# Kernel optimization log

Hardware: AMD Instinct MI355X
Metric: run time of the kernel (lower is better)

Reference implementation:

```python
import jax, jax.numpy as jnp
import numpy as np

NUM_HEADS = 16
ROPE_BASE = 10000.0
LN_EPS = 1e-5


def _rope_tables(seq_len, head_dim, dtype):
    # half-dim angle table: (seq_len, head_dim//2)
    inv_freq = 1.0 / (ROPE_BASE ** (jnp.arange(0, head_dim, 2, dtype=jnp.float32) / head_dim))
    angles = jnp.arange(seq_len, dtype=jnp.float32)[:, None] * inv_freq[None, :]
    return jnp.cos(angles).astype(dtype), jnp.sin(angles).astype(dtype)


def _apply_rope(x, cos, sin):
    # x: (B, H, S, D_h); rotate interleaved (even, odd) dim pairs
    xe = x[..., 0::2]
    xo = x[..., 1::2]
    c = cos[None, None, :, :]
    s = sin[None, None, :, :]
    re = xe * c - xo * s
    ro = xe * s + xo * c
    return jnp.stack([re, ro], axis=-1).reshape(x.shape)


def _layernorm(x, g, b):
    mu = jnp.mean(x, axis=-1, keepdims=True)
    var = jnp.var(x, axis=-1, keepdims=True)
    return (x - mu) * jax.lax.rsqrt(var + LN_EPS) * g + b


def setup_inputs() -> dict:
    key = jax.random.key(0)
    ks = jax.random.split(key, 8)
    B, S, D, F = 2, 2048, 1024, 4096
    sd = lambda fan_in: 1.0 / np.sqrt(fan_in)
    return {
        "x": jax.random.normal(ks[0], (B, S, D), jnp.float32),
        "in_proj_w": jax.random.normal(ks[1], (3 * D, D), jnp.float32) * sd(D),
        "in_proj_b": jnp.zeros((3 * D,), jnp.float32),
        "out_w": jax.random.normal(ks[2], (D, D), jnp.float32) * sd(D),
        "out_b": jnp.zeros((D,), jnp.float32),
        "w1": jax.random.normal(ks[3], (F, D), jnp.float32) * sd(D),
        "b1": jnp.zeros((F,), jnp.float32),
        "w2": jax.random.normal(ks[4], (D, F), jnp.float32) * sd(F),
        "b2": jnp.zeros((D,), jnp.float32),
        "ln1_g": jnp.ones((D,), jnp.float32),
        "ln1_b": jnp.zeros((D,), jnp.float32),
        "ln2_g": jnp.ones((D,), jnp.float32),
        "ln2_b": jnp.zeros((D,), jnp.float32),
    }


def reference(x, in_proj_w, in_proj_b, out_w, out_b, w1, b1, w2, b2,
              ln1_g, ln1_b, ln2_g, ln2_b):
    B, S, D = x.shape
    H = NUM_HEADS
    Dh = D // H
    scale = Dh ** -0.5

    # fused QKV projection
    qkv = x @ in_proj_w.T + in_proj_b  # (B, S, 3D)
    q, k, v = jnp.split(qkv, 3, axis=-1)
    q = q.reshape(B, S, H, Dh).transpose(0, 2, 1, 3)
    k = k.reshape(B, S, H, Dh).transpose(0, 2, 1, 3)
    v = v.reshape(B, S, H, Dh).transpose(0, 2, 1, 3)

    cos, sin = _rope_tables(S, Dh, x.dtype)
    q = _apply_rope(q, cos, sin)
    k = _apply_rope(k, cos, sin)

    # SDPA (no mask, no dropout)
    scores = jnp.einsum('bhqd,bhkd->bhqk', q, k) * scale
    probs = jax.nn.softmax(scores, axis=-1)
    attn = jnp.einsum('bhqk,bhkd->bhqd', probs, v)
    attn = attn.transpose(0, 2, 1, 3).reshape(B, S, D)
    attn_out = attn @ out_w.T + out_b

    # post-norm encoder layer: residual + LN, FFN, residual + LN
    h = _layernorm(x + attn_out, ln1_g, ln1_b)
    ff = jax.nn.relu(h @ w1.T + b1) @ w2.T + b2
    return _layernorm(h + ff, ln2_g, ln2_b)
```

## Files before the change

kernel.cpp:

```cpp
#include <hip/hip_runtime.h>
#include <math.h>

typedef unsigned short u16;
typedef unsigned int u32;
typedef __attribute__((ext_vector_type(8))) __bf16 bf16x8;
typedef __attribute__((ext_vector_type(4))) float f32x4;

#define AS1 __attribute__((address_space(1)))
#define AS3 __attribute__((address_space(3)))

#define B_ 2
#define S_ 2048
#define D_ 1024
#define H_ 16
#define DH_ 64
#define F_ 4096
#define M_ 4096

__device__ __forceinline__ u16 f2b(float f) {
  u32 u = __builtin_bit_cast(u32, f);
  u += 0x7fffu + ((u >> 16) & 1u);
  return (u16)(u >> 16);
}

__device__ __forceinline__ u32 pack2(float a, float b) {
  u16 lo = __builtin_bit_cast(u16, (__bf16)a);
  u16 hi = __builtin_bit_cast(u16, (__bf16)b);
  return (u32)lo | ((u32)hi << 16);
}

__global__ __launch_bounds__(256) void cvt_kernel(const float* __restrict__ in,
                                                  u16* __restrict__ out, int n4) {
  int i = blockIdx.x * 256 + threadIdx.x;
  if (i < n4) {
    float4 v = ((const float4*)in)[i];
    ushort4 o;
    o.x = f2b(v.x); o.y = f2b(v.y); o.z = f2b(v.z); o.w = f2b(v.w);
    ((ushort4*)out)[i] = o;
  }
}

__global__ __launch_bounds__(256) void tables_kernel(float* __restrict__ cosT,
                                                     float* __restrict__ sinT) {
  int idx = blockIdx.x * 256 + threadIdx.x;
  int s = idx >> 5, i = idx & 31;
  float inv = powf(10000.0f, -(float)i / 32.0f);
  float ang = (float)s * inv;
  cosT[idx] = cosf(ang);
  sinT[idx] = sinf(ang);
}

template <bool BIAS, bool RELU, bool SPLIT, typename OutT>
__global__ __launch_bounds__(256) void gemm_bt(const u16* __restrict__ A,
                                               const u16* __restrict__ Bm,
                                               const float* __restrict__ bias,
                                               OutT* __restrict__ C, int M, int N, int K,
                                               int kChunk) {
  __shared__ u16 sA[128 * 32];
  __shared__ u16 sB[128 * 32];
  const int t = threadIdx.x;
  const int w = t >> 6, lane = t & 63;
  const int fr = lane & 15, fg = lane >> 4;
  const int row0 = blockIdx.y * 128, col0 = blockIdx.x * 128;
  const int wr = (w >> 1) * 64, wc = (w & 1) * 64;

  f32x4 acc[4][4] = {};

  const int rA = t >> 2;
  const int jj = ((t & 3) ^ ((t >> 3) & 3)) << 4;
  const int rdswz = ((fg ^ ((fr >> 1) & 3)) << 4);
  const char* aRead = (const char*)sA + (wr + fr) * 64 + rdswz;
  const char* bRead = (const char*)sB + (wc + fr) * 64 + rdswz;

  const int kb = blockIdx.z * kChunk;
  for (int k0 = kb; k0 < kb + kChunk; k0 += 32) {
#pragma unroll
    for (int i = 0; i < 2; ++i) {
      const char* srcA = (const char*)(A + (size_t)(row0 + i * 64 + rA) * K + k0) + jj;
      const char* srcB = (const char*)(Bm + (size_t)(col0 + i * 64 + rA) * K + k0) + jj;
      char* dA = (char*)sA + i * 4096 + w * 1024;
      char* dB = (char*)sB + i * 4096 + w * 1024;
      __builtin_amdgcn_global_load_lds((const AS1 u32*)srcA, (AS3 u32*)dA, 16, 0, 0);
      __builtin_amdgcn_global_load_lds((const AS1 u32*)srcB, (AS3 u32*)dB, 16, 0, 0);
    }
    __syncthreads();

    bf16x8 af[4], bfr[4];
#pragma unroll
    for (int m = 0; m < 4; ++m) af[m] = *(const bf16x8*)(aRead + m * 1024);
#pragma unroll
    for (int n = 0; n < 4; ++n) bfr[n] = *(const bf16x8*)(bRead + n * 1024);
#pragma unroll
    for (int m = 0; m < 4; ++m)
#pragma unroll
      for (int n = 0; n < 4; ++n)
        acc[m][n] = __builtin_amdgcn_mfma_f32_16x16x32_bf16(af[m], bfr[n], acc[m][n], 0, 0, 0);
    __syncthreads();
  }

  OutT* Cp = C;
  if constexpr (SPLIT) Cp = C + (size_t)blockIdx.z * M * N;
#pragma unroll
  for (int m = 0; m < 4; ++m) {
    const int rowb = row0 + wr + m * 16 + fg * 4;
#pragma unroll
    for (int n = 0; n < 4; ++n) {
      const int col = col0 + wc + n * 16 + fr;
      float bv = BIAS ? bias[col] : 0.0f;
      f32x4 c = acc[m][n];
#pragma unroll
      for (int r = 0; r < 4; ++r) {
        float v = c[r] + bv;
        if (RELU) v = fmaxf(v, 0.0f);
        if constexpr (sizeof(OutT) == 2)
          ((u16*)Cp)[(size_t)(rowb + r) * N + col] = f2b(v);
        else
          ((float*)Cp)[(size_t)(rowb + r) * N + col] = v;
      }
    }
  }
}

__global__ __launch_bounds__(256) void rope_kernel(const u16* __restrict__ qkv,
                                                   const float* __restrict__ cosT,
                                                   const float* __restrict__ sinT,
                                                   u16* __restrict__ qr, u16* __restrict__ kr,
                                                   u16* __restrict__ vt) {
  const int bh = blockIdx.x;
  const int b = bh >> 4, h = bh & 15;
  const int s0 = blockIdx.y * 64;
  const int t = threadIdx.x;

#pragma unroll
  for (int part = 0; part < 2; ++part) {
    const u16* src = qkv + (size_t)(b * S_ + s0) * (3 * D_) + part * D_ + h * DH_;
    u16* dst = (part ? kr : qr) + ((size_t)bh * S_ + s0) * DH_;
    const float psc = part ? 1.0f : 0.125f * 1.44269504088896340736f;
    for (int it = 0; it < 8; ++it) {
      int item = it * 256 + t;
      int sl = item >> 5, i = item & 31;
      u32 v = *(const u32*)(src + (size_t)sl * (3 * D_) + 2 * i);
      float xe = __builtin_bit_cast(float, v << 16);
      float xo = __builtin_bit_cast(float, v & 0xffff0000u);
      int s = s0 + sl;
      float c = cosT[s * 32 + i], sn = sinT[s * 32 + i];
      float re = (xe * c - xo * sn) * psc;
      float ro = (xe * sn + xo * c) * psc;
      *(u32*)(dst + (size_t)sl * DH_ + 2 * i) = pack2(re, ro);
    }
  }

  __shared__ u16 tile[64][65];
  const u16* vsrc = qkv + (size_t)(b * S_ + s0) * (3 * D_) + 2 * D_ + h * DH_;
  for (int it = 0; it < 16; ++it) {
    int sl = it * 4 + (t >> 6), dh = t & 63;
    tile[sl][dh] = vsrc[(size_t)sl * (3 * D_) + dh];
  }
  __syncthreads();
  u16* vdst = vt + (size_t)bh * DH_ * S_ + s0;
  for (int it = 0; it < 16; ++it) {
    int dh = it * 4 + (t >> 6), sl = t & 63;
    vdst[(size_t)dh * S_ + sl] = tile[sl][dh];
  }
}

__global__ __launch_bounds__(256) void attn_kernel(const u16* __restrict__ qr,
                                                   const u16* __restrict__ kr,
                                                   const u16* __restrict__ vt,
                                                   u16* __restrict__ attn) {
  __shared__ u16 sK[2][64 * 64];
  __shared__ u16 sV[2][64 * 64];
  __shared__ u16 plds[4][1024];
  const int bh = blockIdx.x;
  const int b = bh >> 4, h = bh & 15;
  const int q0 = blockIdx.y * 64;
  const int t = threadIdx.x, w = t >> 6, lane = t & 63;
  const int fr = lane & 15, fg = lane >> 4;

  const int qrow = q0 + w * 16 + fr;
  const u16* qbase = qr + ((size_t)bh * S_ + qrow) * DH_;
  bf16x8 qf0 = *(const bf16x8*)(qbase + fg * 8);
  bf16x8 qf1 = *(const bf16x8*)(qbase + 32 + fg * 8);

  const char* kByte = (const char*)(kr + (size_t)bh * S_ * DH_);
  const char* vByte = (const char*)(vt + (size_t)bh * DH_ * S_);
  char* pbase = (char*)&plds[w][0];
  const int ci0 = w * 64 + lane;

  f32x4 oacc[4] = {};
  float psum_acc = 0.0f;
  const float M0 = 12.0f;

  auto stage = [&](int bufb, int kt) {
#pragma unroll
    for (int i = 0; i < 2; ++i) {
      int ci = i * 256 + ci0;
      int r = ci >> 3, j = ci & 7;
      int jj = j ^ (r & 7);
      const char* srcK = kByte + (size_t)(kt + r) * 128 + (jj << 4);
      const char* srcV = vByte + (size_t)r * (S_ * 2) + (size_t)kt * 2 + (jj << 4);
      char* dK = (char*)&sK[bufb][0] + i * 4096 + w * 1024;
      char* dV = (char*)&sV[bufb][0] + i * 4096 + w * 1024;
      __builtin_amdgcn_global_load_lds((const AS1 u32*)srcK, (AS3 u32*)dK, 16, 0, 0);
      __builtin_amdgcn_global_load_lds((const AS1 u32*)srcV, (AS3 u32*)dV, 16, 0, 0);
    }
  };

  stage(0, 0);
  __syncthreads();

  int buf = 0;
  for (int kt = 0; kt < S_; kt += 64) {
    if (kt + 64 < S_) stage(buf ^ 1, kt + 64);

    const char* kB = (const char*)&sK[buf][0];
    const char* vB = (const char*)&sV[buf][0];

    f32x4 st[4];
    __builtin_amdgcn_s_setprio(1);
#pragma unroll
    for (int ks = 0; ks < 4; ++ks) {
      const char* rowp = kB + (ks * 16 + fr) * 128;
      bf16x8 kf0 = *(const bf16x8*)(rowp + ((fg ^ (fr & 7)) << 4));
      bf16x8 kf1 = *(const bf16x8*)(rowp + (((fg + 4) ^ (fr & 7)) << 4));
      f32x4 z = {};
      z = __builtin_amdgcn_mfma_f32_16x16x32_bf16(kf0, qf0, z, 0, 0, 0);
      st[ks] = __builtin_amdgcn_mfma_f32_16x16x32_bf16(kf1, qf1, z, 0, 0, 0);
    }
    __builtin_amdgcn_s_setprio(0);

#pragma unroll
    for (int ks = 0; ks < 4; ++ks) {
      float p0 = __builtin_amdgcn_exp2f(st[ks][0] - M0);
      float p1 = __builtin_amdgcn_exp2f(st[ks][1] - M0);
      float p2 = __builtin_amdgcn_exp2f(st[ks][2] - M0);
      float p3 = __builtin_amdgcn_exp2f(st[ks][3] - M0);
      psum_acc += (p0 + p1) + (p2 + p3);
      int wb = fr * 128 + (((ks * 32) | (fg * 8)) ^ ((fr & 7) << 4));
      *(uint2*)(pbase + wb) = make_uint2(pack2(p0, p1), pack2(p2, p3));
    }

    asm volatile("s_waitcnt lgkmcnt(0)" ::: "memory");
    __builtin_amdgcn_sched_barrier(0);

    __builtin_amdgcn_s_setprio(1);
#pragma unroll
    for (int ksub = 0; ksub < 2; ++ksub) {
      int rb = fr * 128 + (((ksub * 64) | (fg * 16)) ^ ((fr & 7) << 4));
      bf16x8 pf = *(const bf16x8*)(pbase + rb);
#pragma unroll
      for (int d = 0; d < 4; ++d) {
        const char* vp = vB + (d * 16 + fr) * 128 + ((((ksub * 4) | fg) ^ (fr & 7)) << 4);
        bf16x8 vf = *(const bf16x8*)vp;
        oacc[d] = __builtin_amdgcn_mfma_f32_16x16x32_bf16(vf, pf, oacc[d], 0, 0, 0);
      }
    }
    __builtin_amdgcn_s_setprio(0);
    __syncthreads();
    buf ^= 1;
  }

  psum_acc += __shfl_xor(psum_acc, 16);
  psum_acc += __shfl_xor(psum_acc, 32);
  const float inv_l = 1.0f / psum_acc;
  u16* obase = attn + (size_t)(b * S_ + q0 + w * 16 + fr) * D_ + h * DH_;
#pragma unroll
  for (int d = 0; d < 4; ++d) {
    ushort4 o4;
    o4.x = f2b(oacc[d][0] * inv_l);
    o4.y = f2b(oacc[d][1] * inv_l);
    o4.z = f2b(oacc[d][2] * inv_l);
    o4.w = f2b(oacc[d][3] * inv_l);
    *(ushort4*)(obase + d * 16 + fg * 4) = o4;
  }
}

template <int NS, bool WRITE_BF16>
__global__ __launch_bounds__(256) void reduce_ln_kernel(const float* __restrict__ parts,
                                                        const float* __restrict__ bias,
                                                        const float* __restrict__ resid,
                                                        const float* __restrict__ gamma,
                                                        const float* __restrict__ beta,
                                                        float* __restrict__ outf,
                                                        u16* __restrict__ outb) {
  const int row = blockIdx.x;
  const int t = threadIdx.x;
  const size_t base = (size_t)row * D_;
  float4 v = ((const float4*)bias)[t];
  {
    const float4 r4 = ((const float4*)(resid + base))[t];
    v.x += r4.x; v.y += r4.y; v.z += r4.z; v.w += r4.w;
  }
#pragma unroll
  for (int s = 0; s < NS; ++s) {
    const float4 p4 = ((const float4*)(parts + (size_t)s * M_ * D_ + base))[t];
    v.x += p4.x; v.y += p4.y; v.z += p4.z; v.w += p4.w;
  }
  float s = v.x + v.y + v.z + v.w;
  float ss = v.x * v.x + v.y * v.y + v.z * v.z + v.w * v.w;
#pragma unroll
  for (int off = 1; off < 64; off <<= 1) {
    s += __shfl_xor(s, off);
    ss += __shfl_xor(ss, off);
  }
  __shared__ float red[8];
  const int w = t >> 6, lane = t & 63;
  if (lane == 0) { red[w] = s; red[4 + w] = ss; }
  __syncthreads();
  s = red[0] + red[1] + red[2] + red[3];
  ss = red[4] + red[5] + red[6] + red[7];
  const float mu = s * (1.0f / D_);
  const float var = ss * (1.0f / D_) - mu * mu;
  const float rstd = rsqrtf(var + 1e-5f);
  const float4 g4 = ((const float4*)gamma)[t];
  const float4 b4 = ((const float4*)beta)[t];
  float4 o;
  o.x = (v.x - mu) * rstd * g4.x + b4.x;
  o.y = (v.y - mu) * rstd * g4.y + b4.y;
  o.z = (v.z - mu) * rstd * g4.z + b4.z;
  o.w = (v.w - mu) * rstd * g4.w + b4.w;
  ((float4*)(outf + base))[t] = o;
  if constexpr (WRITE_BF16) {
    ushort4 ob;
    ob.x = f2b(o.x); ob.y = f2b(o.y); ob.z = f2b(o.z); ob.w = f2b(o.w);
    ((ushort4*)(outb + base))[t] = ob;
  }
}

extern "C" void kernel_launch(void* const* d_in, const int* in_sizes, int n_in,
                              void* d_out, int out_size, void* d_ws, size_t ws_size,
                              hipStream_t stream) {
  const float* x = (const float*)d_in[0];
  const float* in_proj_w = (const float*)d_in[1];
  const float* in_proj_b = (const float*)d_in[2];
  const float* out_w = (const float*)d_in[3];
  const float* out_b = (const float*)d_in[4];
  const float* w1 = (const float*)d_in[5];
  const float* b1 = (const float*)d_in[6];
  const float* w2 = (const float*)d_in[7];
  const float* b2 = (const float*)d_in[8];
  const float* ln1_g = (const float*)d_in[9];
  const float* ln1_b = (const float*)d_in[10];
  const float* ln2_g = (const float*)d_in[11];
  const float* ln2_b = (const float*)d_in[12];

  char* ws = (char*)d_ws;
  u16* wib = (u16*)(ws + 0);
  u16* wob = (u16*)(ws + 6291456);
  u16* w1b = (u16*)(ws + 8388608);
  u16* w2b = (u16*)(ws + 16777216);
  float* cosT = (float*)(ws + 25165824);
  float* sinT = (float*)(ws + 25427968);
  u16* qkvb = (u16*)(ws + 25690112);
  float* part = (float*)(ws + 25690112);
  u16* qrb = (u16*)(ws + 59244544);
  u16* krb = (u16*)(ws + 67633152);
  u16* vtb = (u16*)(ws + 76021760);
  u16* attnb = (u16*)(ws + 84410368);
  u16* ff = (u16*)(ws + 59244544);
  u16* xb = (u16*)(ws + 92798976);
  float* hf = (float*)(ws + 92798976);
  u16* hb = (u16*)(ws + 109576192);
  (void)ws_size; (void)in_sizes; (void)n_in; (void)out_size;

  cvt_kernel<<<4096, 256, 0, stream>>>(x, xb, 1048576);
  cvt_kernel<<<3072, 256, 0, stream>>>(in_proj_w, wib, 786432);
  cvt_kernel<<<1024, 256, 0, stream>>>(out_w, wob, 262144);
  cvt_kernel<<<4096, 256, 0, stream>>>(w1, w1b, 1048576);
  cvt_kernel<<<4096, 256, 0, stream>>>(w2, w2b, 1048576);
  tables_kernel<<<256, 256, 0, stream>>>(cosT, sinT);

  gemm_bt<true, false, false, u16><<<dim3(24, 32), 256, 0, stream>>>(
      xb, wib, in_proj_b, qkvb, M_, 3 * D_, D_, D_);

  rope_kernel<<<dim3(32, 32), 256, 0, stream>>>(qkvb, cosT, sinT, qrb, krb, vtb);

  attn_kernel<<<dim3(32, 32), 256, 0, stream>>>(qrb, krb, vtb, attnb);

  gemm_bt<false, false, true, float><<<dim3(8, 32, 2), 256, 0, stream>>>(
      attnb, wob, nullptr, part, M_, D_, D_, 512);
  reduce_ln_kernel<2, true><<<4096, 256, 0, stream>>>(part, out_b, x, ln1_g, ln1_b, hf, hb);

  gemm_bt<true, true, false, u16><<<dim3(32, 32), 256, 0, stream>>>(
      hb, w1b, b1, ff, M_, F_, D_, D_);

  gemm_bt<false, false, true, float><<<dim3(8, 32, 2), 256, 0, stream>>>(
      ff, w2b, nullptr, part, M_, D_, F_, 2048);
  reduce_ln_kernel<2, false><<<4096, 256, 0, stream>>>(part, b2, hf, ln2_g, ln2_b,
                                                       (float*)d_out, nullptr);
}
```

Baseline: 394.7 us.

## Add 256x256 double-buffered direct-to-LDS GEMM for QKV and FFN1 projections

```diff
diff --git a/kernel.cpp b/kernel.cpp
--- a/kernel.cpp
+++ b/kernel.cpp
@@ -48,6 +48,116 @@
   float ang = (float)s * inv;
   cosT[idx] = cosf(ang);
   sinT[idx] = sinf(ang);
+}
+
+template <bool RELU>
+__global__ __launch_bounds__(512, 2) void gemm256(const u16* __restrict__ A,
+                                                  const u16* __restrict__ Bm,
+                                                  const float* __restrict__ bias,
+                                                  u16* __restrict__ C, int M, int N, int K) {
+  __shared__ u16 sA[2][256 * 64];
+  __shared__ u16 sB[2][256 * 64];
+  const int t = threadIdx.x;
+  const int w = t >> 6, lane = t & 63;
+  const int fr = lane & 15, fg = lane >> 4;
+  const int wm = w >> 2, wn = w & 3;
+
+  const int nwg = gridDim.x * gridDim.y;
+  const int bid = blockIdx.y * gridDim.x + blockIdx.x;
+  const int swz = (bid & 7) * (nwg >> 3) + (bid >> 3);
+  const int bx = swz % gridDim.x, by = swz / gridDim.x;
+  const int row0 = by * 256, col0 = bx * 256;
+
+  f32x4 acc[8][4] = {};
+
+  auto stage_part = [&](int bf, int kt, int p) {
+    const u16* gsrc = (p & 2) ? Bm : A;
+    const int blk0 = (p & 2) ? col0 : row0;
+    u16(*dstT)[256 * 64] = (p & 2) ? sB : sA;
+#pragma unroll
+    for (int l = 0; l < 2; ++l) {
+      int idx = (w * 2 + l) * 64 + lane;
+      int r = ((p & 1) << 7) + (idx >> 3);
+      int j = idx & 7;
+      const char* src = (const char*)(gsrc + (size_t)(blk0 + r) * K + kt * 64) +
+                        (((j ^ (r & 7)) << 4));
+      char* dst = (char*)&dstT[bf][0] + ((p & 1) << 14) + (w * 2 + l) * 1024;
+      __builtin_amdgcn_global_load_lds((const AS1 u32*)src, (AS3 u32*)dst, 16, 0, 0);
+    }
+  };
+
+  const int NT = K >> 6;
+#pragma unroll
+  for (int p = 0; p < 4; ++p) stage_part(0, 0, p);
+
+  int bufc = 0;
+  for (int kt = 0; kt < NT; ++kt) {
+    const int nx = bufc ^ 1;
+    bf16x8 bfr[4][2];
+#pragma unroll
+    for (int ph = 0; ph < 4; ++ph) {
+      if (ph == 0) {
+        if (kt + 1 < NT) {
+          stage_part(nx, kt + 1, 0);
+          asm volatile("s_waitcnt vmcnt(2)" ::: "memory");
+        } else {
+          asm volatile("s_waitcnt vmcnt(0)" ::: "memory");
+        }
+        __builtin_amdgcn_s_barrier();
+        __builtin_amdgcn_sched_barrier(0);
+#pragma unroll
+        for (int n = 0; n < 4; ++n)
+#pragma unroll
+          for (int kh = 0; kh < 2; ++kh) {
+            int br = wn * 64 + n * 16 + fr;
+            bfr[n][kh] = *(const bf16x8*)((const char*)&sB[bufc][0] + br * 128 +
+                                          (((kh * 4 + fg) ^ (br & 7)) << 4));
+          }
+      } else {
+        if (kt + 1 < NT) stage_part(nx, kt + 1, ph);
+      }
+      bf16x8 af[2][2];
+#pragma unroll
+      for (int mm = 0; mm < 2; ++mm)
+#pragma unroll
+        for (int kh = 0; kh < 2; ++kh) {
+          int ar = wm * 128 + (ph * 2 + mm) * 16 + fr;
+          af[mm][kh] = *(const bf16x8*)((const char*)&sA[bufc][0] + ar * 128 +
+                                        (((kh * 4 + fg) ^ (ar & 7)) << 4));
+        }
+      if (ph != 0) __builtin_amdgcn_s_barrier();
+      __builtin_amdgcn_s_setprio(1);
+#pragma unroll
+      for (int mm = 0; mm < 2; ++mm)
+#pragma unroll
+        for (int n = 0; n < 4; ++n)
+#pragma unroll
+          for (int kh = 0; kh < 2; ++kh)
+            acc[ph * 2 + mm][n] = __builtin_amdgcn_mfma_f32_16x16x32_bf16(
+                af[mm][kh], bfr[n][kh], acc[ph * 2 + mm][n], 0, 0, 0);
+      __builtin_amdgcn_s_setprio(0);
+      __builtin_amdgcn_s_barrier();
+    }
+    bufc = nx;
+  }
+
+  float bs[4];
+#pragma unroll
+  for (int n = 0; n < 4; ++n) bs[n] = bias[col0 + wn * 64 + n * 16 + fr];
+#pragma unroll
+  for (int m = 0; m < 8; ++m) {
+    const int rowb = row0 + wm * 128 + m * 16 + fg * 4;
+#pragma unroll
+    for (int n = 0; n < 4; ++n) {
+      const int col = col0 + wn * 64 + n * 16 + fr;
+#pragma unroll
+      for (int rr = 0; rr < 4; ++rr) {
+        float v = acc[m][n][rr] + bs[n];
+        if (RELU) v = fmaxf(v, 0.0f);
+        C[(size_t)(rowb + rr) * N + col] = f2b(v);
+      }
+    }
+  }
 }
 
 template <bool BIAS, bool RELU, bool SPLIT, typename OutT>
@@ -370,8 +480,7 @@
   cvt_kernel<<<4096, 256, 0, stream>>>(w2, w2b, 1048576);
   tables_kernel<<<256, 256, 0, stream>>>(cosT, sinT);
 
-  gemm_bt<true, false, false, u16><<<dim3(24, 32), 256, 0, stream>>>(
-      xb, wib, in_proj_b, qkvb, M_, 3 * D_, D_, D_);
+  gemm256<false><<<dim3(12, 16), 512, 0, stream>>>(xb, wib, in_proj_b, qkvb, M_, 3 * D_, D_);
 
   rope_kernel<<<dim3(32, 32), 256, 0, stream>>>(qkvb, cosT, sinT, qrb, krb, vtb);
 
@@ -381,8 +490,7 @@
       attnb, wob, nullptr, part, M_, D_, D_, 512);
   reduce_ln_kernel<2, true><<<4096, 256, 0, stream>>>(part, out_b, x, ln1_g, ln1_b, hf, hb);
 
-  gemm_bt<true, true, false, u16><<<dim3(32, 32), 256, 0, stream>>>(
-      hb, w1b, b1, ff, M_, F_, D_, D_);
+  gemm256<true><<<dim3(16, 16), 512, 0, stream>>>(hb, w1b, b1, ff, M_, F_, D_);
 
   gemm_bt<false, false, true, float><<<dim3(8, 32, 2), 256, 0, stream>>>(
       ff, w2b, nullptr, part, M_, D_, F_, 2048);
```

Result: slower. 412.2 us (+4.4%).
